# Kernel optimization log

Measured on AMD Instinct MI355X. Metric: run time of the kernel, lower is better.

The kernel has to match this reference:

```python
import jax, jax.numpy as jnp
import numpy as np

NCLASS = 21  # num_classes from init
EPS = 1e-6


def setup_inputs() -> dict:
    key = jax.random.key(0)
    k1, k2 = jax.random.split(key)
    feats = jax.random.normal(k1, (8, 256, 64, 64), dtype=jnp.float32)
    masks = jax.random.randint(k2, (8, 256, 256), 0, NCLASS, dtype=jnp.int32)
    return {"feats": feats, "masks": masks}


def reference(feats, masks):
    # feats: [B, C, h, w] float; masks: [B, H, W] int labels
    B, C, _, _ = feats.shape
    H, W = masks.shape[-2:]
    # F.interpolate(..., mode='bilinear', align_corners=False) == half-pixel bilinear resize
    f = jax.image.resize(feats, (B, C, H, W), method="bilinear")  # [B,C,H,W]
    f_flat = f.reshape(B, C, H * W)  # [B,C,P]

    # labels > nclass (e.g. 255 ignore) are clamped to the dump bucket `nclass`;
    # pixels with label == nclass are excluded (one_hot drops out-of-range rows).
    lbl = jnp.where(masks > NCLASS, NCLASS, masks).reshape(B, H * W)  # [B,P]
    onehot = jax.nn.one_hot(lbl, NCLASS, dtype=f.dtype)  # [B,P,K], dump bucket -> all zeros

    # segment-reduce: per-image per-class feature sums and pixel counts
    sums = jnp.einsum("bcp,bpk->bkc", f_flat, onehot)  # [B,K,C]
    counts = onehot.sum(axis=1)  # [B,K]
    per_img = sums / (counts[..., None] + EPS)  # [B,K,C]; absent classes -> ~0, matching torch loop skip
    prototypes = per_img.mean(axis=0)  # [K,C] (sum over batch / b)
    return prototypes
```

## Files before the change

### kernel.cpp

```cpp
#include <hip/hip_runtime.h>

#define NK 21
#define NC 256
#define NSRC 64
#define NOUT 256
#define NB 8
#define EPS 1e-6f

__global__ __launch_bounds__(256, 4)
void proto_main(const float* __restrict__ feats,
                const int* __restrict__ masks,
                float* __restrict__ psum,
                float* __restrict__ pcnt) {
  __shared__ __align__(16) float Wl[NK * 32];
  __shared__ int hist[NK];

  const int tid = threadIdx.x;
  const int r0 = blockIdx.x;
  const int b = blockIdx.y;
  const int z = blockIdx.z;

  const float4* fbase = (const float4*)(
      feats + ((size_t)(b * NC + tid) << 12) + (size_t)r0 * 64 + 32 * z);
  const float4 f0 = fbase[0], f1 = fbase[1], f2 = fbase[2], f3 = fbase[3];
  const float4 f4 = fbase[4], f5 = fbase[5], f6 = fbase[6], f7 = fbase[7];

  for (int i = tid; i < NK * 32; i += 256) Wl[i] = 0.f;
  if (tid < NK) hist[tid] = 0;
  __syncthreads();

  int ylo = 4 * r0 - 2; if (ylo < 0) ylo = 0;
  int yhi = 4 * r0 + 5; if (yhi > NOUT - 1) yhi = NOUT - 1;
  const int xlo = z ? 126 : 0;
  const int npix = (yhi - ylo + 1) * 130;
  const int own_lo = 4 * r0;

  for (int i = tid; i < npix; i += 256) {
    const int x = xlo + i % 130;
    const int y = ylo + i / 130;
    const int lbl = masks[((size_t)b * NOUT + y) * NOUT + x];
    if ((unsigned)lbl < NK) {
      const int ry = y >> 2, py = y & 3;
      const int j0y = (py < 2) ? ry - 1 : ry;
      const float fy = (py == 0) ? 0.625f : (py == 1) ? 0.875f
                     : (py == 2) ? 0.125f : 0.375f;
      const int rx = x >> 2, px = x & 3;
      const int j0x = (px < 2) ? rx - 1 : rx;
      const float fx = (px == 0) ? 0.625f : (px == 1) ? 0.875f
                     : (px == 2) ? 0.125f : 0.375f;

      const int cx0 = (j0x < 0) ? 0 : j0x;
      const int cx1 = (j0x + 1 > NSRC - 1) ? NSRC - 1 : j0x + 1;
      const float wx0 = 1.f - fx, wx1 = fx;
      const int ry0 = (j0y < 0) ? 0 : j0y;
      const int ry1 = (j0y + 1 > NSRC - 1) ? NSRC - 1 : j0y + 1;
      const float wy0 = 1.f - fy, wy1 = fy;

      float* Wk = &Wl[lbl * 32];
      if (ry0 == r0) {
        if ((cx0 >> 5) == z) atomicAdd(&Wk[cx0 & 31], wy0 * wx0);
        if ((cx1 >> 5) == z) atomicAdd(&Wk[cx1 & 31], wy0 * wx1);
      }
      if (ry1 == r0) {
        if ((cx0 >> 5) == z) atomicAdd(&Wk[cx0 & 31], wy1 * wx0);
        if ((cx1 >> 5) == z) atomicAdd(&Wk[cx1 & 31], wy1 * wx1);
      }
      if (y >= own_lo && y < own_lo + 4 && (x >> 7) == z)
        atomicAdd(&hist[lbl], 1);
    }
  }
  __syncthreads();

  float acc[NK];
#pragma unroll
  for (int k = 0; k < NK; ++k) acc[k] = 0.f;

  const float4* wb = (const float4*)Wl;
#pragma unroll
  for (int k = 0; k < NK; ++k) {
    const float4 w0 = wb[k * 8 + 0], w1 = wb[k * 8 + 1];
    const float4 w2 = wb[k * 8 + 2], w3 = wb[k * 8 + 3];
    float a = acc[k];
    a = fmaf(f0.x, w0.x, a); a = fmaf(f0.y, w0.y, a);
    a = fmaf(f0.z, w0.z, a); a = fmaf(f0.w, w0.w, a);
    a = fmaf(f1.x, w1.x, a); a = fmaf(f1.y, w1.y, a);
    a = fmaf(f1.z, w1.z, a); a = fmaf(f1.w, w1.w, a);
    a = fmaf(f2.x, w2.x, a); a = fmaf(f2.y, w2.y, a);
    a = fmaf(f2.z, w2.z, a); a = fmaf(f2.w, w2.w, a);
    a = fmaf(f3.x, w3.x, a); a = fmaf(f3.y, w3.y, a);
    a = fmaf(f3.z, w3.z, a); a = fmaf(f3.w, w3.w, a);
    acc[k] = a;
  }
#pragma unroll
  for (int k = 0; k < NK; ++k) {
    const float4 w4 = wb[k * 8 + 4], w5 = wb[k * 8 + 5];
    const float4 w6 = wb[k * 8 + 6], w7 = wb[k * 8 + 7];
    float a = acc[k];
    a = fmaf(f4.x, w4.x, a); a = fmaf(f4.y, w4.y, a);
    a = fmaf(f4.z, w4.z, a); a = fmaf(f4.w, w4.w, a);
    a = fmaf(f5.x, w5.x, a); a = fmaf(f5.y, w5.y, a);
    a = fmaf(f5.z, w5.z, a); a = fmaf(f5.w, w5.w, a);
    a = fmaf(f6.x, w6.x, a); a = fmaf(f6.y, w6.y, a);
    a = fmaf(f6.z, w6.z, a); a = fmaf(f6.w, w6.w, a);
    a = fmaf(f7.x, w7.x, a); a = fmaf(f7.y, w7.y, a);
    a = fmaf(f7.z, w7.z, a); a = fmaf(f7.w, w7.w, a);
    acc[k] = a;
  }

#pragma unroll
  for (int k = 0; k < NK; ++k)
    atomicAdd(&psum[((size_t)b * NK + k) * NC + tid], acc[k]);
  if (tid < NK) atomicAdd(&pcnt[(size_t)b * NK + tid], (float)hist[tid]);
}

__global__ __launch_bounds__(256)
void proto_final(const float* __restrict__ psum,
                 const float* __restrict__ pcnt,
                 float* __restrict__ out) {
  const int k = blockIdx.x;
  const int c = threadIdx.x;
  float a = 0.f;
#pragma unroll
  for (int b = 0; b < NB; ++b)
    a += psum[((size_t)b * NK + k) * NC + c] / (pcnt[(size_t)b * NK + k] + EPS);
  out[(size_t)k * NC + c] = a * 0.125f;
}

extern "C" void kernel_launch(void* const* d_in, const int* in_sizes, int n_in,
                              void* d_out, int out_size, void* d_ws, size_t ws_size,
                              hipStream_t stream) {
  const float* feats = (const float*)d_in[0];
  const int* masks = (const int*)d_in[1];
  float* out = (float*)d_out;

  float* psum = (float*)d_ws;
  float* pcnt = psum + (size_t)NB * NK * NC;
  const size_t zbytes = ((size_t)NB * NK * NC + (size_t)NB * NK) * 4;

  hipMemsetAsync(d_ws, 0, zbytes, stream);
  proto_main<<<dim3(64, NB, 2), 256, 0, stream>>>(feats, masks, psum, pcnt);
  proto_final<<<dim3(NK), 256, 0, stream>>>(psum, pcnt, out);
}
```

Measured before the change: 110.6 us.

## Replace global atomics with per-slice partial buffers and two-stage reduction

Each block now writes its per-class partial sums and counts to its own slot in a slice-indexed workspace instead of atomically adding into a shared per-image buffer. This removes the memset and global atomic contention. A two-kernel reduction then sums 128 slices per image and averages over the batch. LDS float atomics are switched to a relaxed, workgroup-scoped fetch_add intrinsic. The trade-off is a larger workspace (~22 MB of partials to write and read back) and one extra kernel launch.

```diff
diff --git a/kernel.cpp b/kernel.cpp
--- a/kernel.cpp
+++ b/kernel.cpp
@@ -5,7 +5,12 @@
 #define NSRC 64
 #define NOUT 256
 #define NB 8
+#define NSL 128
 #define EPS 1e-6f
+
+__device__ __forceinline__ void lds_fadd(float* p, float v) {
+  __hip_atomic_fetch_add(p, v, __ATOMIC_RELAXED, __HIP_MEMORY_SCOPE_WORKGROUP);
+}
 
 __global__ __launch_bounds__(256, 4)
 void proto_main(const float* __restrict__ feats,
@@ -58,12 +63,12 @@
 
       float* Wk = &Wl[lbl * 32];
       if (ry0 == r0) {
-        if ((cx0 >> 5) == z) atomicAdd(&Wk[cx0 & 31], wy0 * wx0);
-        if ((cx1 >> 5) == z) atomicAdd(&Wk[cx1 & 31], wy0 * wx1);
+        if ((cx0 >> 5) == z) lds_fadd(&Wk[cx0 & 31], wy0 * wx0);
+        if ((cx1 >> 5) == z) lds_fadd(&Wk[cx1 & 31], wy0 * wx1);
       }
       if (ry1 == r0) {
-        if ((cx0 >> 5) == z) atomicAdd(&Wk[cx0 & 31], wy1 * wx0);
-        if ((cx1 >> 5) == z) atomicAdd(&Wk[cx1 & 31], wy1 * wx1);
+        if ((cx0 >> 5) == z) lds_fadd(&Wk[cx0 & 31], wy1 * wx0);
+        if ((cx1 >> 5) == z) lds_fadd(&Wk[cx1 & 31], wy1 * wx1);
       }
       if (y >= own_lo && y < own_lo + 4 && (x >> 7) == z)
         atomicAdd(&hist[lbl], 1);
@@ -107,23 +112,39 @@
     acc[k] = a;
   }
 
+  const int sl = r0 * 2 + z;
+  float* dst = psum + ((size_t)(b * NSL + sl) * NK) * NC + tid;
 #pragma unroll
-  for (int k = 0; k < NK; ++k)
-    atomicAdd(&psum[((size_t)b * NK + k) * NC + tid], acc[k]);
-  if (tid < NK) atomicAdd(&pcnt[(size_t)b * NK + tid], (float)hist[tid]);
+  for (int k = 0; k < NK; ++k) dst[k * NC] = acc[k];
+  if (tid < NK) pcnt[(size_t)(b * NSL + sl) * NK + tid] = (float)hist[tid];
 }
 
 __global__ __launch_bounds__(256)
-void proto_final(const float* __restrict__ psum,
-                 const float* __restrict__ pcnt,
-                 float* __restrict__ out) {
+void proto_finalA(const float* __restrict__ psum,
+                  const float* __restrict__ pcnt,
+                  float* __restrict__ tmp) {
+  const int k = blockIdx.x;
+  const int b = blockIdx.y;
+  const int c = threadIdx.x;
+  float s = 0.f, cnt = 0.f;
+#pragma unroll
+  for (int sl = 0; sl < NSL; ++sl) {
+    s += psum[((size_t)(b * NSL + sl) * NK + k) * NC + c];
+    cnt += pcnt[(size_t)(b * NSL + sl) * NK + k];
+  }
+  tmp[((size_t)b * NK + k) * NC + c] = s / (cnt + EPS) * 0.125f;
+}
+
+__global__ __launch_bounds__(256)
+void proto_finalB(const float* __restrict__ tmp,
+                  float* __restrict__ out) {
   const int k = blockIdx.x;
   const int c = threadIdx.x;
   float a = 0.f;
 #pragma unroll
   for (int b = 0; b < NB; ++b)
-    a += psum[((size_t)b * NK + k) * NC + c] / (pcnt[(size_t)b * NK + k] + EPS);
-  out[(size_t)k * NC + c] = a * 0.125f;
+    a += tmp[((size_t)b * NK + k) * NC + c];
+  out[(size_t)k * NC + c] = a;
 }
 
 extern "C" void kernel_launch(void* const* d_in, const int* in_sizes, int n_in,
@@ -134,10 +155,10 @@
   float* out = (float*)d_out;
 
   float* psum = (float*)d_ws;
-  float* pcnt = psum + (size_t)NB * NK * NC;
-  const size_t zbytes = ((size_t)NB * NK * NC + (size_t)NB * NK) * 4;
+  float* pcnt = psum + (size_t)NB * NSL * NK * NC;
+  float* tmp = pcnt + (size_t)NB * NSL * NK;
 
-  hipMemsetAsync(d_ws, 0, zbytes, stream);
   proto_main<<<dim3(64, NB, 2), 256, 0, stream>>>(feats, masks, psum, pcnt);
-  proto_final<<<dim3(NK), 256, 0, stream>>>(psum, pcnt, out);
+  proto_finalA<<<dim3(NK, NB), 256, 0, stream>>>(psum, pcnt, tmp);
+  proto_finalB<<<dim3(NK), 256, 0, stream>>>(tmp, out);
 }
```

After: 101.4 us. 1.09x faster.
